# Performance work log

Hardware: AMD Instinct MI355X
Metric: run time of the kernel (lower is better)

Reference implementation:

```python
import jax, jax.numpy as jnp
import numpy as np

B, L, N, FA, FB, D, OUT, R, T = 128, 128, 6, 39, 10, 200, 1, 3, 2
MB = 256  # num bonds per molecule
NEG = -9e8


def setup_inputs():
    key = jax.random.key(0)
    ks = iter(jax.random.split(key, 64))
    def rn(shape, sc=0.05):
        return jax.random.normal(next(ks), shape, dtype=jnp.float32) * sc
    inp = {}
    inp['atom_list'] = jax.random.normal(next(ks), (B, L, FA), dtype=jnp.float32)
    inp['bond_list'] = jax.random.normal(next(ks), (B, MB, FB), dtype=jnp.float32)
    inp['atom_degree_list'] = jax.random.randint(next(ks), (B, L, N), 0, L, dtype=jnp.int32)
    inp['bond_degree_list'] = jax.random.randint(next(ks), (B, L, N), 0, MB, dtype=jnp.int32)
    inp['atom_mask'] = jnp.ones((B, L), dtype=jnp.float32)
    # parameters (torch Linear: y = x @ W + b with W stored here as [in, out])
    inp['W_atom'] = rn((FA, D)); inp['b_atom'] = rn((D,))
    inp['W_nei'] = rn((FA + FB, D)); inp['b_nei'] = rn((D,))
    inp['W_align'] = rn((R, 2 * D, 1)); inp['b_align'] = rn((R, 1))
    inp['W_attend'] = rn((R, D, D)); inp['b_attend'] = rn((R, D))
    # GRUCell weights, torch layout [3D, D], gate order r,z,n
    inp['Wih'] = rn((R, 3 * D, D)); inp['Whh'] = rn((R, 3 * D, D))
    inp['bih'] = rn((R, 3 * D)); inp['bhh'] = rn((R, 3 * D))
    inp['W_mol_align'] = rn((2 * D, 1)); inp['b_mol_align'] = rn((1,))
    inp['W_mol_attend'] = rn((D, D)); inp['b_mol_attend'] = rn((D,))
    inp['mWih'] = rn((3 * D, D)); inp['mWhh'] = rn((3 * D, D))
    inp['mbih'] = rn((3 * D,)); inp['mbhh'] = rn((3 * D,))
    inp['W_metric'] = rn((2 * D, D)); inp['b_metric'] = rn((D,))
    inp['W_out'] = rn((D, OUT)); inp['b_out'] = rn((OUT,))
    return inp


def _gather(feat, idx):
    # feat [B, M, F], idx [B, L, N] -> [B, L, N, F]
    b, l, n = idx.shape
    g = jnp.take_along_axis(feat, idx.reshape(b, l * n)[..., None], axis=1)
    return g.reshape(b, l, n, feat.shape[-1])


def _gru(x, h, Wih, Whh, bih, bhh):
    gi = x @ Wih.T + bih
    gh = h @ Whh.T + bhh
    ir, iz, inn = jnp.split(gi, 3, axis=-1)
    hr, hz, hn = jnp.split(gh, 3, axis=-1)
    r = jax.nn.sigmoid(ir + hr)
    z = jax.nn.sigmoid(iz + hz)
    n = jnp.tanh(inn + r * hn)
    return (1.0 - z) * n + z * h


def reference(atom_list, bond_list, atom_degree_list, bond_degree_list, atom_mask,
              W_atom, b_atom, W_nei, b_nei, W_align, b_align, W_attend, b_attend,
              Wih, Whh, bih, bhh, W_mol_align, b_mol_align, W_mol_attend, b_mol_attend,
              mWih, mWhh, mbih, mbhh, W_metric, b_metric, W_out, b_out):
    lrelu = jax.nn.leaky_relu
    b, l, _ = atom_list.shape
    atom_feature = lrelu(atom_list @ W_atom + b_atom)          # [B,L,D]
    atom_nei = _gather(atom_list, atom_degree_list)            # [B,L,N,FA]
    bond_nei = _gather(bond_list, bond_degree_list)            # [B,L,N,FB]
    nei = lrelu(jnp.concatenate([atom_nei, bond_nei], -1) @ W_nei + b_nei)  # [B,L,N,D]

    pad = (atom_degree_list == l - 1)
    attend_mask = (~pad).astype(jnp.float32)[..., None]        # [B,L,N,1]
    softmax_mask = jnp.where(pad, NEG, 0.0)[..., None]         # [B,L,N,1]

    h = atom_feature
    cur = atom_feature
    for r in range(R):
        if r > 0:
            nei = _gather(cur, atom_degree_list)
        exp = jnp.broadcast_to(cur[:, :, None, :], nei.shape)
        align = lrelu(jnp.concatenate([exp, nei], -1) @ W_align[r] + b_align[r])
        w = jax.nn.softmax(align + softmax_mask, axis=-2) * attend_mask
        trans = nei @ W_attend[r] + b_attend[r]
        ctx = jax.nn.elu(jnp.sum(w * trans, axis=-2))          # [B,L,D]
        h = _gru(ctx.reshape(-1, D), h.reshape(-1, D), Wih[r], Whh[r], bih[r], bhh[r]).reshape(b, l, D)
        cur = jax.nn.relu(h)

    am = atom_mask[..., None]                                   # [B,L,1]
    mol_feature = jnp.sum(cur * am, axis=-2)                    # [B,D]
    act_mol = jax.nn.relu(mol_feature)
    mol_softmax_mask = jnp.where(am == 0.0, NEG, 0.0)           # [B,L,1]
    for _ in range(T):
        exp = jnp.broadcast_to(act_mol[:, None, :], cur.shape)
        score = lrelu(jnp.concatenate([exp, cur], -1) @ W_mol_align + b_mol_align)
        w = jax.nn.softmax(score + mol_softmax_mask, axis=-2) * am
        trans = cur @ W_mol_attend + b_mol_attend
        ctx = jax.nn.elu(jnp.sum(w * trans, axis=-2))           # [B,D]
        mol_feature = _gru(ctx, mol_feature, mWih, mWhh, mbih, mbhh)
        act_mol = jax.nn.relu(mol_feature)

    dd = jnp.float32(R - 2)  # leaked python loop var `d` in the original
    feat = jnp.concatenate([mol_feature, mol_feature + dd], -1)
    return (feat @ W_metric + b_metric) @ W_out + b_out


if __name__ == '__main__':
    out = reference(**setup_inputs())
    print(out.shape)
```

## Files before the change

### kernel.cpp

```cpp
#include <hip/hip_runtime.h>
#include <hip/hip_bf16.h>
#include <math.h>
#include <string.h>

#define B_ 128
#define L_ 128
#define N_ 6
#define FA_ 39
#define FB_ 10
#define D_ 200
#define MB_ 256
#define R_ 3
#define T_ 2
#define NEGV -9e8f
#define BL_ (B_*L_)
#define G3D_ (3*D_)
#define FP32TAG 0x3F800000u
#define KP 416
#define NP 896
#define NP2 1024
#define KC 224
#define NC 256

typedef __hip_bfloat16 bf16;
typedef __attribute__((ext_vector_type(8))) short short8;
typedef __attribute__((ext_vector_type(4))) float f32x4;

__device__ __forceinline__ float b2f(const bf16 x){ return __bfloat162float(x); }
__device__ __forceinline__ unsigned short f2b(float v){ bf16 t = __float2bfloat16(v); return *reinterpret_cast<unsigned short*>(&t); }
__device__ __forceinline__ float bu2f(unsigned short u){ unsigned x = ((unsigned)u)<<16; float f; memcpy(&f,&x,4); return f; }
__device__ __forceinline__ float lo2f(unsigned x){ unsigned y = x<<16; float f; memcpy(&f,&y,4); return f; }
__device__ __forceinline__ float hi2f(unsigned x){ unsigned y = x & 0xffff0000u; float f; memcpy(&f,&y,4); return f; }
__device__ __forceinline__ float lreluf(float x){ return x>=0.f ? x : 0.01f*x; }
__device__ __forceinline__ float eluf(float x){ return x>0.f ? x : expm1f(x); }
__device__ __forceinline__ float sigmf(float x){ return 1.f/(1.f+expf(-x)); }

#define NSEG 14
struct CvtArgs { const void* src[NSEG]; int ofs[NSEG+1]; };

#define PREPB_N (R_*NP2*KP)
#define PREPW_N (R_*NC*KC)
#define PREPM_N (D_*G3D_)
#define PREPG_N (2*PREPM_N)
#define PREPT_N 40000
#define PREPE_N 80000
#define CONV_N 23989
#define XHPAD_N (BL_*16)
#define CPAD_N (BL_*24)
#define AROWS (BL_ + B_*MB_)
#define A_N (AROWS*64)
#define BI_N (448*64)

struct PrepArgs {
    CvtArgs cvt;
    const void *Wih, *Whh, *Watt, *mWih, *mWhh, *Wmt, *Wme;
    const void *bond, *Wnei, *atom, *Watom;
    float* conv;
    unsigned short *B2t, *WatT, *WGi, *WGh, *WmtT, *WmeT, *XH, *A16, *Bi16, *cur16;
    const unsigned* amtag;
    int ew_total;
};

__device__ __forceinline__ float ldd(const void* p, size_t i, bool f32){
    return f32 ? ((const float*)p)[i] : b2f(((const bf16*)p)[i]);
}

__global__ void __launch_bounds__(256) k_prep(PrepArgs A){
    bool f32 = (*A.amtag == FP32TAG);
    int i = blockIdx.x*256 + (int)threadIdx.x;
    if (i >= A.ew_total) return;
    if (i < CONV_N){
        int s = 0;
        while (i >= A.cvt.ofs[s+1]) s++;
        A.conv[i] = ldd(A.cvt.src[s], i - A.cvt.ofs[s], f32);
        return;
    }
    int i2 = i - CONV_N;
    if (i2 < PREPB_N){
        int kk = i2 % KP;
        int rest = i2 / KP;
        int c = rest % NP2;
        int r = rest / NP2;
        int g = c >> 8, n = c & 255;
        float v = 0.f;
        if (n < 200){
            if (g <= 1){
                int j = g*200 + n;
                if (kk < 200) v = ldd(A.Wih, ((size_t)(r*G3D_ + j))*D_ + kk, f32);
                else if (kk < 400) v = ldd(A.Whh, ((size_t)(r*G3D_ + j))*D_ + (kk-200), f32);
            } else if (g == 2){
                if (kk < 200) v = ldd(A.Wih, ((size_t)(r*G3D_ + 400 + n))*D_ + kk, f32);
            } else {
                if (kk >= 200 && kk < 400) v = ldd(A.Whh, ((size_t)(r*G3D_ + 400 + n))*D_ + (kk-200), f32);
            }
        }
        A.B2t[i2] = f2b(v);
        return;
    }
    int i3 = i2 - PREPB_N;
    if (i3 < PREPW_N){
        int kk = i3 % KC;
        int rest = i3 / KC;
        int n = rest % NC;
        int r = rest / NC;
        float v = 0.f;
        if (kk < 200 && n < 200) v = ldd(A.Watt, ((size_t)r*D_ + kk)*D_ + n, f32);
        A.WatT[i3] = f2b(v);
        return;
    }
    int i4 = i3 - PREPW_N;
    if (i4 < PREPG_N){
        int half = i4 / PREPM_N;
        int s = i4 - half*PREPM_N;
        (half ? A.WGh : A.WGi)[s] = f2b(ldd(half ? A.mWhh : A.mWih, s, f32));
        return;
    }
    int i5 = i4 - PREPG_N;
    if (i5 < PREPT_N){
        int k = i5 / 200, d = i5 % 200;
        A.WmtT[(size_t)d*200 + k] = f2b(ldd(A.Wmt, i5, f32));
        return;
    }
    int i6 = i5 - PREPT_N;
    if (i6 < PREPE_N){
        int k = i6 / 200, d = i6 % 200;
        A.WmeT[(size_t)d*400 + k] = f2b(ldd(A.Wme, i6, f32));
        return;
    }
    int i7 = i6 - PREPE_N;
    if (i7 < XHPAD_N){
        int al = i7 >> 4, j = i7 & 15;
        A.XH[(size_t)al*KP + 400 + j] = 0;
        return;
    }
    int i7b = i7 - XHPAD_N;
    if (i7b < CPAD_N){
        int al = i7b / 24, j = i7b % 24;
        A.cur16[(size_t)al*KC + 200 + j] = 0;
        return;
    }
    int i8 = i7b - CPAD_N;
    if (i8 < A_N){
        int row = i8 >> 6, k = i8 & 63;
        float v = 0.f;
        if (row < BL_){
            if (k < FA_) v = ldd(A.atom, (size_t)row*FA_ + k, f32);
        } else {
            int rb = row - BL_;
            if (k >= FA_ && k < FA_+FB_) v = ldd(A.bond, (size_t)rb*FB_ + (k-FA_), f32);
        }
        A.A16[i8] = f2b(v);
        return;
    }
    int i9 = i8 - A_N;
    if (i9 < BI_N){
        int n = i9 >> 6, k = i9 & 63;
        float v = 0.f;
        if (n < 200){
            if (k < FA_) v = ldd(A.Watom, (size_t)k*D_ + n, f32);
        } else if (n < 400){
            if (k < FA_+FB_) v = ldd(A.Wnei, (size_t)k*D_ + (n-200), f32);
        }
        A.Bi16[i9] = f2b(v);
    }
}

__global__ void __launch_bounds__(256) k_initmm(const unsigned short* __restrict__ A16,
        const unsigned short* __restrict__ Bi16,
        const void* __restrict__ batom, const void* __restrict__ bnei,
        unsigned short* __restrict__ XH, unsigned short* __restrict__ P16,
        unsigned short* __restrict__ Q16, const unsigned* __restrict__ amtag){
    __shared__ unsigned short As[128][40];
    __shared__ unsigned short Bs[64][40];
    bool f32 = (*amtag == FP32TAG);
    int tid = threadIdx.x;
    int mt = (int)blockIdx.x / 7, nt = (int)blockIdx.x % 7;
    int m0 = mt*128, n0 = nt*64;
    if (m0 >= BL_ && n0 + 64 <= 200) return;
    int lane = tid & 63, wv = tid >> 6;
    int quad = lane >> 4, lm = lane & 15;
    f32x4 acc[2][4];
    #pragma unroll
    for (int a=0;a<2;a++)
        #pragma unroll
        for (int b=0;b<4;b++) acc[a][b] = (f32x4){0.f,0.f,0.f,0.f};
    for (int ks = 0; ks < 2; ks++){
        int r0_ = tid >> 2, c0 = (tid & 3) * 8;
        int r1_ = (tid + 256) >> 2, c1 = ((tid + 256) & 3) * 8;
        uint4 a0 = *(const uint4*)&A16[(size_t)(m0 + r0_)*64 + ks*32 + c0];
        uint4 a1 = *(const uint4*)&A16[(size_t)(m0 + r1_)*64 + ks*32 + c1];
        uint4 b0 = *(const uint4*)&Bi16[(size_t)(n0 + (tid >> 2))*64 + ks*32 + (tid & 3)*8];
        __syncthreads();
        *(uint4*)&As[r0_][c0] = a0;
        *(uint4*)&As[r1_][c1] = a1;
        *(uint4*)&Bs[tid >> 2][(tid & 3)*8] = b0;
        __syncthreads();
        short8 av0 = *(const short8*)&As[wv*32 + lm][quad*8];
        short8 av1 = *(const short8*)&As[wv*32 + 16 + lm][quad*8];
        #pragma unroll
        for (int ns=0; ns<4; ns++){
            short8 bv = *(const short8*)&Bs[ns*16 + lm][quad*8];
            acc[0][ns] = __builtin_amdgcn_mfma_f32_16x16x32_bf16(av0, bv, acc[0][ns], 0,0,0);
            acc[1][ns] = __builtin_amdgcn_mfma_f32_16x16x32_bf16(av1, bv, acc[1][ns], 0,0,0);
        }
    }
    #pragma unroll
    for (int ms=0; ms<2; ms++)
      #pragma unroll
      for (int ns=0; ns<4; ns++){
        int n = n0 + ns*16 + lm;
        #pragma unroll
        for (int i=0;i<4;i++){
            int row = m0 + wv*32 + ms*16 + quad*4 + i;
            float v = acc[ms][ns][i];
            if (row < BL_){
                if (n < 200){
                    XH[(size_t)row*KP + 200 + n] = f2b(lreluf(v + ldd(batom, n, f32)));
                } else if (n < 400){
                    P16[(size_t)row*D_ + (n-200)] = f2b(v + ldd(bnei, n-200, f32));
                }
            } else if (n >= 200 && n < 400){
                Q16[(size_t)(row-BL_)*D_ + (n-200)] = f2b(v);
            }
        }
      }
}

__global__ void __launch_bounds__(256) k_attn(
        const unsigned short* __restrict__ cur16, const unsigned short* __restrict__ XH,
        const float* __restrict__ s1, const float* __restrict__ tb,
        const int* __restrict__ adl, const int* __restrict__ bdl,
        const unsigned short* __restrict__ P16, const unsigned short* __restrict__ Q16,
        const float* __restrict__ W_align, const float* __restrict__ b_align, int r,
        unsigned short* __restrict__ wnei, float* __restrict__ wsum){
    int bid = blockIdx.x;
    int mol = bid & (B_-1), chunk = bid >> 7;
    int wv = threadIdx.x >> 6, lane = threadIdx.x & 63;
    int al = mol*L_ + chunk*4 + wv;
    __shared__ float s_nei[4][N_][D_];

    int idxn[N_]; bool pad[N_];
    #pragma unroll
    for (int n=0;n<N_;n++){ idxn[n] = adl[al*N_ + n]; pad[n] = (idxn[n] == L_-1); }

    float s2[N_];
    float s1v;
    if (r == 0){
        const float* Wab = W_align + D_;
        float acc[N_+1];
        #pragma unroll
        for (int n=0;n<N_+1;n++) acc[n] = 0.f;
        #pragma unroll
        for (int n=0;n<N_;n++){
            int bd = bdl[al*N_ + n];
            const unsigned short* Prow = P16 + ((size_t)mol*L_ + idxn[n])*D_;
            const unsigned short* Qrow = Q16 + ((size_t)mol*MB_ + bd)*D_;
            for (int d=lane; d<D_; d+=64){
                float v = lreluf(bu2f(Prow[d]) + bu2f(Qrow[d]));
                s_nei[wv][n][d] = v;
                acc[n] += v * Wab[d];
            }
        }
        for (int d=lane; d<D_; d+=64)
            acc[N_] += bu2f(XH[(size_t)al*KP + 200 + d]) * W_align[d];
        #pragma unroll
        for (int o=32;o>0;o>>=1)
            #pragma unroll
            for (int n=0;n<N_+1;n++) acc[n] += __shfl_xor(acc[n],o);
        #pragma unroll
        for (int n=0;n<N_;n++) s2[n] = acc[n];
        s1v = acc[N_];
    } else {
        float tmp = 0.f;
        if (lane < N_) tmp = tb[mol*L_ + idxn[lane]];
        #pragma unroll
        for (int n=0;n<N_;n++) s2[n] = __shfl(tmp, n);
        s1v = s1[al];
    }

    float bav = b_align[r];
    float a[N_]; float mx = -1e30f;
    #pragma unroll
    for (int n=0;n<N_;n++){
        float v = lreluf(s1v + s2[n] + bav);
        if (pad[n]) v += NEGV;
        a[n] = v; mx = fmaxf(mx, v);
    }
    float w[N_]; float se = 0.f;
    #pragma unroll
    for (int n=0;n<N_;n++){ float e = expf(a[n]-mx); w[n]=e; se += e; }
    float inv = 1.f/se; float wsv = 0.f;
    #pragma unroll
    for (int n=0;n<N_;n++){ w[n] = pad[n] ? 0.f : w[n]*inv; wsv += w[n]; }

    if (r == 0){
        for (int d=lane; d<D_; d+=64){
            float acc = 0.f;
            #pragma unroll
            for (int n=0;n<N_;n++) acc += w[n] * s_nei[wv][n][d];
            wnei[(size_t)al*KC + d] = f2b(acc);
        }
    } else {
        for (int d=lane; d<D_; d+=64){
            float acc = 0.f;
            #pragma unroll
            for (int n=0;n<N_;n++) acc += w[n] * bu2f(cur16[((size_t)mol*L_ + idxn[n])*KC + d]);
            wnei[(size_t)al*KC + d] = f2b(acc);
        }
    }
    if (lane < 24) wnei[(size_t)al*KC + 200 + lane] = 0;
    if (lane==0) wsum[al] = wsv;
}

__global__ void __launch_bounds__(256) k_ctxmfma(const unsigned short* __restrict__ Wn,
        const float* __restrict__ wsum, const unsigned short* __restrict__ WatT,
        const float* __restrict__ bias, int r, unsigned short* __restrict__ XH,
        float* __restrict__ s1, float* __restrict__ tb, float* __restrict__ curdot){
    __shared__ unsigned short As[128][40];
    __shared__ unsigned short Bs[64][40];
    int tid = threadIdx.x;
    int m0 = ((int)blockIdx.x & 127) * 128;
    int n0 = ((int)blockIdx.x >> 7) * 64;
    if (n0 == 0 && tid < 128){
        int row = m0 + tid;
        s1[row] = 0.f; tb[row] = 0.f;
        if (r == R_-1) curdot[row] = 0.f;
        #pragma unroll
        for (int j=0;j<16;j++) XH[(size_t)row*KP + 400 + j] = 0;
    }
    const unsigned short* Bt = WatT + (size_t)r*NC*KC;
    int lane = tid & 63, wv = tid >> 6;
    int quad = lane >> 4, lm = lane & 15;
    f32x4 acc[2][4];
    #pragma unroll
    for (int a=0;a<2;a++)
        #pragma unroll
        for (int b=0;b<4;b++) acc[a][b] = (f32x4){0.f,0.f,0.f,0.f};
    for (int ks = 0; ks < 7; ks++){
        int r0_ = tid >> 2, c0 = (tid & 3) * 8;
        int r1_ = (tid + 256) >> 2, c1 = ((tid + 256) & 3) * 8;
        uint4 a0 = *(const uint4*)&Wn[(size_t)(m0 + r0_)*KC + ks*32 + c0];
        uint4 a1 = *(const uint4*)&Wn[(size_t)(m0 + r1_)*KC + ks*32 + c1];
        uint4 b0 = *(const uint4*)&Bt[(size_t)(n0 + (tid >> 2))*KC + ks*32 + (tid & 3)*8];
        __syncthreads();
        *(uint4*)&As[r0_][c0] = a0;
        *(uint4*)&As[r1_][c1] = a1;
        *(uint4*)&Bs[tid >> 2][(tid & 3)*8] = b0;
        __syncthreads();
        short8 av0 = *(const short8*)&As[wv*32 + lm][quad*8];
        short8 av1 = *(const short8*)&As[wv*32 + 16 + lm][quad*8];
        #pragma unroll
        for (int ns=0; ns<4; ns++){
            short8 bv = *(const short8*)&Bs[ns*16 + lm][quad*8];
            acc[0][ns] = __builtin_amdgcn_mfma_f32_16x16x32_bf16(av0, bv, acc[0][ns], 0,0,0);
            acc[1][ns] = __builtin_amdgcn_mfma_f32_16x16x32_bf16(av1, bv, acc[1][ns], 0,0,0);
        }
    }
    #pragma unroll
    for (int ms=0; ms<2; ms++)
      #pragma unroll
      for (int ns=0; ns<4; ns++){
        int n = n0 + ns*16 + lm;
        if (n < 200){
            float bv = bias[r*D_ + n];
            #pragma unroll
            for (int i=0;i<4;i++){
                int row = m0 + wv*32 + ms*16 + quad*4 + i;
                float v = acc[ms][ns][i] + wsum[row]*bv;
                XH[(size_t)row*KP + n] = f2b(eluf(v));
            }
        }
      }
}

__global__ void __launch_bounds__(256, 2) k_gemm2(
        const unsigned short* __restrict__ XHr, unsigned short* __restrict__ XHw,
        const unsigned short* __restrict__ B2t, unsigned short* __restrict__ cur16,
        const float* __restrict__ bih, const float* __restrict__ bhh,
        const float* __restrict__ W_align, const float* __restrict__ Wma,
        float* __restrict__ s1, float* __restrict__ tb, float* __restrict__ curdot,
        int r){
    __shared__ unsigned short As[128][40];
    __shared__ unsigned short Bs[256][40];
    __shared__ float s_ab[4][128][2];
    int tid = threadIdx.x;
    int m0 = ((int)blockIdx.x & 127) * 128;
    int ds = (int)blockIdx.x >> 7;
    const unsigned short* Bt = B2t + (size_t)r*NP2*KP;
    int lane = tid & 63, wn = tid >> 6;
    int quad = lane >> 4, lm = lane & 15;
    f32x4 acc[8][4];
    #pragma unroll
    for (int a=0;a<8;a++)
        #pragma unroll
        for (int b=0;b<4;b++) acc[a][b] = (f32x4){0.f,0.f,0.f,0.f};
    int ar = tid >> 2, ac = (tid & 3) * 8;
    for (int ks = 0; ks < 13; ks++){
        uint4 a0 = *(const uint4*)&XHr[(size_t)(m0 + ar)*KP + ks*32 + ac];
        uint4 a1 = *(const uint4*)&XHr[(size_t)(m0 + 64 + ar)*KP + ks*32 + ac];
        uint4 bq[4];
        #pragma unroll
        for (int q=0;q<4;q++)
            bq[q] = *(const uint4*)&Bt[(size_t)(q*256 + ds*64 + ar)*KP + ks*32 + ac];
        __syncthreads();
        *(uint4*)&As[ar][ac] = a0;
        *(uint4*)&As[64 + ar][ac] = a1;
        #pragma unroll
        for (int q=0;q<4;q++) *(uint4*)&Bs[q*64 + ar][ac] = bq[q];
        __syncthreads();
        short8 bv[4];
        #pragma unroll
        for (int g=0;g<4;g++) bv[g] = *(const short8*)&Bs[g*64 + wn*16 + lm][quad*8];
        #pragma unroll
        for (int mm=0; mm<8; mm++){
            short8 av = *(const short8*)&As[mm*16 + lm][quad*8];
            #pragma unroll
            for (int g=0;g<4;g++)
                acc[mm][g] = __builtin_amdgcn_mfma_f32_16x16x32_bf16(av, bv[g], acc[mm][g], 0,0,0);
        }
    }
    const float* bi = bih + r*G3D_;
    const float* bh = bhh + r*G3D_;
    const float* Wa = W_align + (r+1)*2*D_;
    bool last = (r == R_-1);
    int d = ds*64 + wn*16 + lm;
    bool dok = (d < 200);
    float bir=0.f,biz=0.f,bin=0.f,bhr=0.f,bhz=0.f,bhn=0.f,wa1=0.f,wa2=0.f;
    if (dok){
        bir=bi[d]; biz=bi[D_+d]; bin=bi[2*D_+d];
        bhr=bh[d]; bhz=bh[D_+d]; bhn=bh[2*D_+d];
        wa1 = last ? Wma[D_+d] : Wa[d];
        wa2 = last ? 0.f : Wa[D_+d];
    }
    #pragma unroll
    for (int mm=0; mm<8; mm++){
        float pa[4] = {0.f,0.f,0.f,0.f}, pb[4] = {0.f,0.f,0.f,0.f};
        if (dok){
            #pragma unroll
            for (int i=0;i<4;i++){
                int row = m0 + mm*16 + quad*4 + i;
                float rsum = acc[mm][0][i];
                float zsum = acc[mm][1][i];
                float gin  = acc[mm][2][i];
                float ghn  = acc[mm][3][i];
                float rr = sigmf(rsum + bir + bhr);
                float zz = sigmf(zsum + biz + bhz);
                float nn = tanhf(gin + bin + rr*(ghn + bhn));
                size_t hx = (size_t)row*KP + 200 + d;
                float hv = bu2f(XHr[hx]);
                float hn = (1.f-zz)*nn + zz*hv;
                XHw[hx] = f2b(hn);
                float cv = fmaxf(hn, 0.f);
                cur16[(size_t)row*KC + d] = f2b(cv);
                pa[i] += cv * wa1;
                pb[i] += cv * wa2;
            }
        }
        #pragma unroll
        for (int o=1;o<16;o<<=1){
            #pragma unroll
            for (int i=0;i<4;i++){ pa[i] += __shfl_xor(pa[i],o); pb[i] += __shfl_xor(pb[i],o); }
        }
        if (lm == 0){
            #pragma unroll
            for (int i=0;i<4;i++){
                int lr = mm*16 + quad*4 + i;
                s_ab[wn][lr][0] = pa[i];
                s_ab[wn][lr][1] = pb[i];
            }
        }
    }
    __syncthreads();
    if (tid < 128){
        int row = m0 + tid;
        float a1 = (s_ab[0][tid][0] + s_ab[1][tid][0]) + (s_ab[2][tid][0] + s_ab[3][tid][0]);
        float a2 = (s_ab[0][tid][1] + s_ab[1][tid][1]) + (s_ab[2][tid][1] + s_ab[3][tid][1]);
        if (last) atomicAdd(&curdot[row], a1);
        else { atomicAdd(&s1[row], a1); atomicAdd(&tb[row], a2); }
    }
}

__device__ __forceinline__ float brSum(float v, float* s_red){
    for (int o=32;o>0;o>>=1) v += __shfl_xor(v,o);
    int lane = threadIdx.x & 63, wid = threadIdx.x >> 6;
    __syncthreads();
    if (lane==0) s_red[wid] = v;
    __syncthreads();
    float r = 0.f;
    int nw = blockDim.x >> 6;
    for (int i=0;i<nw;i++) r += s_red[i];
    return r;
}

__device__ __forceinline__ float dot200(const unsigned short* __restrict__ wrow,
                                        const float* __restrict__ v){
    const uint4* wp = (const uint4*)wrow;
    float a0=0.f, a1=0.f;
    #pragma unroll
    for (int kk=0; kk<25; kk++){
        uint4 u = wp[kk];
        f32x4 A = *(const f32x4*)&v[8*kk];
        f32x4 Bv = *(const f32x4*)&v[8*kk+4];
        a0 += A[0]*lo2f(u.x) + A[1]*hi2f(u.x);
        a1 += A[2]*lo2f(u.y) + A[3]*hi2f(u.y);
        a0 += Bv[0]*lo2f(u.z) + Bv[1]*hi2f(u.z);
        a1 += Bv[2]*lo2f(u.w) + Bv[3]*hi2f(u.w);
    }
    return a0 + a1;
}

__global__ void __launch_bounds__(512, 1) k_mol(const unsigned short* __restrict__ cur16,
    const float* __restrict__ curdot, const float* __restrict__ atom_mask,
    const float* __restrict__ Wma, const float* __restrict__ bma,
    const unsigned short* __restrict__ WmtT, const float* __restrict__ bmt,
    const unsigned short* __restrict__ WGi, const unsigned short* __restrict__ WGh,
    const float* __restrict__ mbih, const float* __restrict__ mbhh,
    const unsigned short* __restrict__ WmeT, const float* __restrict__ bme,
    const float* __restrict__ Wout, const float* __restrict__ bout,
    void* __restrict__ out, const unsigned* __restrict__ amtag){
    int b = blockIdx.x, tid = threadIdx.x;
    int wv = tid >> 6, lane = tid & 63;
    int dq = tid & 255, cq = tid >> 8;
    __shared__ unsigned short s_cur[L_*KC];
    __shared__ float s_am[L_], s_neg[L_], s_cd[L_];
    __shared__ float s_wp[4][L_];
    __shared__ __attribute__((aligned(16))) float s_mf[D_];
    __shared__ __attribute__((aligned(16))) float s_act[D_];
    __shared__ __attribute__((aligned(16))) float s_wc[D_];
    __shared__ __attribute__((aligned(16))) float s_ctx[D_];
    __shared__ __attribute__((aligned(16))) float s_mf2[2*D_];
    __shared__ float s_gi[G3D_], s_gh[G3D_];
    __shared__ float s_wma[D_], s_bmt[D_], s_bi[G3D_], s_bh[G3D_];
    __shared__ float s_part[2][256];
    __shared__ float s_red[8];
    __shared__ float s_wsm;
    const uint4* src = (const uint4*)(cur16 + (size_t)b*L_*KC);
    for (int i = tid; i < L_*KC/8; i += 512) ((uint4*)s_cur)[i] = src[i];
    if (tid < L_){
        float am = atom_mask[b*L_ + tid];
        s_am[tid] = am;
        s_neg[tid] = (am == 0.f) ? NEGV : 0.f;
        s_cd[tid] = curdot[b*L_ + tid];
    }
    if (tid < D_){ s_wma[tid] = Wma[tid]; s_bmt[tid] = bmt[tid]; }
    for (int j = tid; j < G3D_; j += 512){
        s_bi[j] = mbih[j];
        s_bh[j] = mbhh[j];
    }
    __syncthreads();
    {
        float a0 = 0.f, a1 = 0.f;
        if (dq < D_)
            for (int l=cq*64; l<cq*64+64; l+=2){
                a0 += bu2f(s_cur[l*KC + dq]) * s_am[l];
                a1 += bu2f(s_cur[(l+1)*KC + dq]) * s_am[l+1];
            }
        s_part[cq][dq] = a0 + a1;
        __syncthreads();
        if (tid < D_){
            float v = s_part[0][tid] + s_part[1][tid];
            s_mf[tid] = v; s_act[tid] = fmaxf(v, 0.f);
        }
        __syncthreads();
    }
    float bma0 = bma[0];
    #pragma unroll 1
    for (int t=0;t<T_;t++){
        if (wv < 4){
            float a = s_act[lane]*s_wma[lane] + s_act[lane+64]*s_wma[lane+64];
            a += s_act[lane+128]*s_wma[lane+128];
            if (lane < 8) a += s_act[lane+192]*s_wma[lane+192];
            #pragma unroll
            for (int o=32;o>0;o>>=1) a += __shfl_xor(a,o);
            float sc0 = lreluf(a + s_cd[lane] + bma0) + s_neg[lane];
            float sc1 = lreluf(a + s_cd[lane+64] + bma0) + s_neg[lane+64];
            float m = fmaxf(sc0, sc1);
            #pragma unroll
            for (int o=32;o>0;o>>=1) m = fmaxf(m, __shfl_xor(m,o));
            float e0 = expf(sc0 - m), e1 = expf(sc1 - m);
            float s = e0 + e1;
            #pragma unroll
            for (int o=32;o>0;o>>=1) s += __shfl_xor(s,o);
            float inv = 1.f/s;
            float w0 = e0*inv*s_am[lane], w1 = e1*inv*s_am[lane+64];
            float ws = w0 + w1;
            #pragma unroll
            for (int o=32;o>0;o>>=1) ws += __shfl_xor(ws,o);
            s_wp[wv][lane] = w0; s_wp[wv][lane+64] = w1;
            if (tid == 0) s_wsm = ws;
            if (tid < D_){
                float acc = 0.f;
                #pragma unroll 16
                for (int l=0; l<L_; l++)
                    acc += s_wp[wv][l] * bu2f(s_cur[l*KC + tid]);
                s_wc[tid] = acc;
            }
        } else {
            int h = tid - 256;
            #pragma unroll 1
            for (int rr=0; rr<3; rr++){
                int row = h + rr*256;
                if (row < G3D_)
                    s_gh[row] = dot200(WGh + (size_t)row*D_, s_mf);
                __builtin_amdgcn_sched_barrier(0);
            }
        }
        __syncthreads();
        if (tid < D_){
            float acc = dot200(WmtT + (size_t)tid*D_, s_wc);
            s_ctx[tid] = eluf(acc + s_wsm * s_bmt[tid]);
        }
        __syncthreads();
        {
            #pragma unroll 1
            for (int rr=0; rr<2; rr++){
                int row = tid + rr*512;
                if (row < G3D_)
                    s_gi[row] = dot200(WGi + (size_t)row*D_, s_ctx);
                __builtin_amdgcn_sched_barrier(0);
            }
        }
        __syncthreads();
        if (tid < D_){
            int d = tid;
            float rr = sigmf(s_gi[d] + s_bi[d] + s_gh[d] + s_bh[d]);
            float zz = sigmf(s_gi[D_+d] + s_bi[D_+d] + s_gh[D_+d] + s_bh[D_+d]);
            float nn = tanhf(s_gi[2*D_+d] + s_bi[2*D_+d] + rr*(s_gh[2*D_+d] + s_bh[2*D_+d]));
            float nm = (1.f-zz)*nn + zz*s_mf[d];
            s_mf[d] = nm; s_act[d] = fmaxf(nm, 0.f);
        }
        __syncthreads();
        __builtin_amdgcn_sched_barrier(0);
    }
    const float dd = (float)(R_ - 2);
    if (tid < 2*D_) s_mf2[tid] = (tid < D_) ? s_mf[tid] : s_mf[tid - D_] + dd;
    __syncthreads();
    float p2 = 0.f;
    if (tid < D_){
        const uint4* wp = (const uint4*)(WmeT + (size_t)tid*400);
        float a0=0.f, a1=0.f;
        #pragma unroll
        for (int kk=0; kk<50; kk++){
            uint4 u = wp[kk];
            f32x4 wA = *(const f32x4*)&s_mf2[8*kk];
            f32x4 wB = *(const f32x4*)&s_mf2[8*kk+4];
            a0 += wA[0]*lo2f(u.x) + wA[1]*hi2f(u.x);
            a1 += wA[2]*lo2f(u.y) + wA[3]*hi2f(u.y);
            a0 += wB[0]*lo2f(u.z) + wB[1]*hi2f(u.z);
            a1 += wB[2]*lo2f(u.w) + wB[3]*hi2f(u.w);
        }
        p2 = (a0 + a1 + bme[tid]) * Wout[tid];
    }
    float o = brSum(p2, s_red);
    if (tid==0){
        o += bout[0];
        if (*amtag == FP32TAG) ((float*)out)[b] = o;
        else ((bf16*)out)[b] = __float2bfloat16(o);
    }
}

extern "C" void kernel_launch(void* const* d_in, const int* in_sizes, int n_in,
                              void* d_out, int out_size, void* d_ws, size_t ws_size,
                              hipStream_t stream) {
    const int* adl = (const int*)d_in[2];
    const int* bdl = (const int*)d_in[3];
    const unsigned* amtag = (const unsigned*)d_in[4];

    static const int srcidx[NSEG] = {4,9,10,12,15,16,17,18,20,23,24,26,27,28};
    static const int segsz[NSEG]  = {16384,1200,3,600,1800,1800,400,1,200,600,600,200,200,1};
    CvtArgs ca;
    int ofs[NSEG+1]; ofs[0] = 0;
    for (int i=0;i<NSEG;i++){ ca.src[i] = d_in[srcidx[i]]; ca.ofs[i] = ofs[i]; ofs[i+1] = ofs[i] + segsz[i]; }
    ca.ofs[NSEG] = ofs[NSEG];

    float* ws   = (float*)d_ws;
    float* conv = ws;
    unsigned short* XHa   = (unsigned short*)(conv + 24000);
    unsigned short* B2t   = XHa + (size_t)BL_*KP;
    unsigned short* WatT  = B2t + PREPB_N;
    unsigned short* WGi   = WatT + PREPW_N;
    unsigned short* WGh   = WGi + PREPM_N;
    unsigned short* WmtT  = WGh + PREPM_N;
    unsigned short* WmeT  = WmtT + PREPT_N;
    unsigned short* Bi16  = WmeT + PREPE_N;
    unsigned short* cur16 = Bi16 + BI_N;
    unsigned short* creg  = cur16 + (size_t)BL_*KC;
    unsigned short* A16  = creg;
    unsigned short* wnei = creg;
    unsigned short* Q16  = creg + (size_t)BL_*KC;
    unsigned short* P16  = Q16 + (size_t)B_*MB_*D_;
    unsigned short* XHb  = Q16;
    float* s1     = (float*)(creg + (size_t)BL_*NP);
    float* tb     = s1 + BL_;
    float* wsum   = tb + BL_;
    float* curdot = wsum + BL_;

    const float* c_amask = conv + ofs[0];
    const float* c_Walign= conv + ofs[1];
    const float* c_balign= conv + ofs[2];
    const float* c_batt  = conv + ofs[3];
    const float* c_bih   = conv + ofs[4];
    const float* c_bhh   = conv + ofs[5];
    const float* c_Wma   = conv + ofs[6];
    const float* c_bma   = conv + ofs[7];
    const float* c_bmt   = conv + ofs[8];
    const float* c_mbih  = conv + ofs[9];
    const float* c_mbhh  = conv + ofs[10];
    const float* c_bme   = conv + ofs[11];
    const float* c_Wout  = conv + ofs[12];
    const float* c_bout  = conv + ofs[13];

    PrepArgs A;
    A.cvt = ca;
    A.Wih = d_in[13]; A.Whh = d_in[14]; A.Watt = d_in[11];
    A.mWih = d_in[21]; A.mWhh = d_in[22]; A.Wmt = d_in[19]; A.Wme = d_in[25];
    A.bond = d_in[1]; A.Wnei = d_in[7]; A.atom = d_in[0]; A.Watom = d_in[5];
    A.conv = conv;
    A.B2t = B2t; A.WatT = WatT; A.WGi = WGi; A.WGh = WGh; A.WmtT = WmtT; A.WmeT = WmeT;
    A.XH = XHa; A.A16 = A16; A.Bi16 = Bi16; A.cur16 = cur16;
    A.amtag = amtag;
    A.ew_total = CONV_N + PREPB_N + PREPW_N + PREPG_N + PREPT_N + PREPE_N
               + XHPAD_N + CPAD_N + A_N + BI_N;

    k_prep<<<(A.ew_total + 255)/256, 256, 0, stream>>>(A);
    k_initmm<<<(AROWS/128)*7, 256, 0, stream>>>(A16, Bi16, d_in[6], d_in[8],
                                                XHa, P16, Q16, amtag);

    for (int r=0; r<R_; r++){
        unsigned short* XHr = (r & 1) ? XHb : XHa;
        unsigned short* XHw = (r & 1) ? XHa : XHb;
        k_attn<<<BL_/4, 256, 0, stream>>>(cur16, XHa, s1, tb, adl, bdl, P16, Q16,
                                          c_Walign, c_balign, r, wnei, wsum);
        k_ctxmfma<<<(BL_/128)*(NC/64), 256, 0, stream>>>(wnei, wsum, WatT, c_batt, r, XHr,
                                                         s1, tb, curdot);
        k_gemm2<<<512, 256, 0, stream>>>(XHr, XHw, B2t, cur16, c_bih, c_bhh,
                                         c_Walign, c_Wma, s1, tb, curdot, r);
    }

    k_mol<<<B_, 512, 0, stream>>>(cur16, curdot, c_amask, c_Wma, c_bma, WmtT, c_bmt,
                                  WGi, WGh, c_mbih, c_mbhh, WmeT, c_bme, c_Wout, c_bout,
                                  d_out, amtag);
}
```

Before: 437.6 us.

## Halve GEMM2 M-tile and register-prefetch next K slice in fused GRU kernel

The GRU gate GEMM kernel now uses 64-row M tiles instead of 128, doubling the grid to 1024 blocks and raising the occupancy hint to 3 blocks per CU. The global loads for the next K slice are issued into registers right after the shared-memory store, so they overlap the MFMA work on the current slice. The block index mapping also changes so that the four N-slices of one M tile sit in adjacent blocks. In exchange, each B tile is reloaded twice as often, so there is less reuse of the weight tile per block.

After: 514.0 us. 17.4% more time.

```diff
diff --git a/kernel.cpp b/kernel.cpp
--- a/kernel.cpp
+++ b/kernel.cpp
@@ -373,46 +373,51 @@
       }
 }
 
-__global__ void __launch_bounds__(256, 2) k_gemm2(
+__global__ void __launch_bounds__(256, 3) k_gemm2(
         const unsigned short* __restrict__ XHr, unsigned short* __restrict__ XHw,
         const unsigned short* __restrict__ B2t, unsigned short* __restrict__ cur16,
         const float* __restrict__ bih, const float* __restrict__ bhh,
         const float* __restrict__ W_align, const float* __restrict__ Wma,
         float* __restrict__ s1, float* __restrict__ tb, float* __restrict__ curdot,
         int r){
-    __shared__ unsigned short As[128][40];
+    __shared__ unsigned short As[64][40];
     __shared__ unsigned short Bs[256][40];
-    __shared__ float s_ab[4][128][2];
+    __shared__ float s_ab[4][64][2];
     int tid = threadIdx.x;
-    int m0 = ((int)blockIdx.x & 127) * 128;
-    int ds = (int)blockIdx.x >> 7;
+    int m0 = ((int)blockIdx.x >> 2) * 64;
+    int ds = (int)blockIdx.x & 3;
     const unsigned short* Bt = B2t + (size_t)r*NP2*KP;
     int lane = tid & 63, wn = tid >> 6;
     int quad = lane >> 4, lm = lane & 15;
-    f32x4 acc[8][4];
-    #pragma unroll
-    for (int a=0;a<8;a++)
+    f32x4 acc[4][4];
+    #pragma unroll
+    for (int a=0;a<4;a++)
         #pragma unroll
         for (int b=0;b<4;b++) acc[a][b] = (f32x4){0.f,0.f,0.f,0.f};
     int ar = tid >> 2, ac = (tid & 3) * 8;
+    uint4 pa = *(const uint4*)&XHr[(size_t)(m0 + ar)*KP + ac];
+    uint4 pb[4];
+    #pragma unroll
+    for (int q=0;q<4;q++)
+        pb[q] = *(const uint4*)&Bt[(size_t)(q*256 + ds*64 + ar)*KP + ac];
     for (int ks = 0; ks < 13; ks++){
-        uint4 a0 = *(const uint4*)&XHr[(size_t)(m0 + ar)*KP + ks*32 + ac];
-        uint4 a1 = *(const uint4*)&XHr[(size_t)(m0 + 64 + ar)*KP + ks*32 + ac];
-        uint4 bq[4];
-        #pragma unroll
-        for (int q=0;q<4;q++)
-            bq[q] = *(const uint4*)&Bt[(size_t)(q*256 + ds*64 + ar)*KP + ks*32 + ac];
-        __syncthreads();
-        *(uint4*)&As[ar][ac] = a0;
-        *(uint4*)&As[64 + ar][ac] = a1;
-        #pragma unroll
-        for (int q=0;q<4;q++) *(uint4*)&Bs[q*64 + ar][ac] = bq[q];
-        __syncthreads();
+        __syncthreads();
+        *(uint4*)&As[ar][ac] = pa;
+        #pragma unroll
+        for (int q=0;q<4;q++) *(uint4*)&Bs[q*64 + ar][ac] = pb[q];
+        __syncthreads();
+        if (ks < 12){
+            int ko = (ks+1)*32 + ac;
+            pa = *(const uint4*)&XHr[(size_t)(m0 + ar)*KP + ko];
+            #pragma unroll
+            for (int q=0;q<4;q++)
+                pb[q] = *(const uint4*)&Bt[(size_t)(q*256 + ds*64 + ar)*KP + ko];
+        }
         short8 bv[4];
         #pragma unroll
         for (int g=0;g<4;g++) bv[g] = *(const short8*)&Bs[g*64 + wn*16 + lm][quad*8];
         #pragma unroll
-        for (int mm=0; mm<8; mm++){
+        for (int mm=0; mm<4; mm++){
             short8 av = *(const short8*)&As[mm*16 + lm][quad*8];
             #pragma unroll
             for (int g=0;g<4;g++)
@@ -433,8 +438,8 @@
         wa2 = last ? 0.f : Wa[D_+d];
     }
     #pragma unroll
-    for (int mm=0; mm<8; mm++){
-        float pa[4] = {0.f,0.f,0.f,0.f}, pb[4] = {0.f,0.f,0.f,0.f};
+    for (int mm=0; mm<4; mm++){
+        float pa_[4] = {0.f,0.f,0.f,0.f}, pb_[4] = {0.f,0.f,0.f,0.f};
         if (dok){
             #pragma unroll
             for (int i=0;i<4;i++){
@@ -452,26 +457,26 @@
                 XHw[hx] = f2b(hn);
                 float cv = fmaxf(hn, 0.f);
                 cur16[(size_t)row*KC + d] = f2b(cv);
-                pa[i] += cv * wa1;
-                pb[i] += cv * wa2;
+                pa_[i] += cv * wa1;
+                pb_[i] += cv * wa2;
             }
         }
         #pragma unroll
         for (int o=1;o<16;o<<=1){
             #pragma unroll
-            for (int i=0;i<4;i++){ pa[i] += __shfl_xor(pa[i],o); pb[i] += __shfl_xor(pb[i],o); }
+            for (int i=0;i<4;i++){ pa_[i] += __shfl_xor(pa_[i],o); pb_[i] += __shfl_xor(pb_[i],o); }
         }
         if (lm == 0){
             #pragma unroll
             for (int i=0;i<4;i++){
                 int lr = mm*16 + quad*4 + i;
-                s_ab[wn][lr][0] = pa[i];
-                s_ab[wn][lr][1] = pb[i];
+                s_ab[wn][lr][0] = pa_[i];
+                s_ab[wn][lr][1] = pb_[i];
             }
         }
     }
     __syncthreads();
-    if (tid < 128){
+    if (tid < 64){
         int row = m0 + tid;
         float a1 = (s_ab[0][tid][0] + s_ab[1][tid][0]) + (s_ab[2][tid][0] + s_ab[3][tid][0]);
         float a2 = (s_ab[0][tid][1] + s_ab[1][tid][1]) + (s_ab[2][tid][1] + s_ab[3][tid][1]);
@@ -733,8 +738,8 @@
                                           c_Walign, c_balign, r, wnei, wsum);
         k_ctxmfma<<<(BL_/128)*(NC/64), 256, 0, stream>>>(wnei, wsum, WatT, c_batt, r, XHr,
                                                          s1, tb, curdot);
-        k_gemm2<<<512, 256, 0, stream>>>(XHr, XHw, B2t, cur16, c_bih, c_bhh,
-                                         c_Walign, c_Wma, s1, tb, curdot, r);
+        k_gemm2<<<1024, 256, 0, stream>>>(XHr, XHw, B2t, cur16, c_bih, c_bhh,
+                                          c_Walign, c_Wma, s1, tb, curdot, r);
     }
 
     k_mol<<<B_, 512, 0, stream>>>(cur16, curdot, c_amask, c_Wma, c_bma, WmtT, c_bmt,
```
